# Performance work log

Measured on AMD Instinct MI355X. Metric: run time of the kernel, lower is better.

Reference implementation:

```python
import jax, jax.numpy as jnp
import numpy as np

B, CIN, H, W = 16, 20, 256, 256
WIDTH, M1, M2, NLAYERS, FC_HID, COUT = 64, 16, 16, 4, 128, 20


def setup_inputs() -> dict:
    key = jax.random.key(0)
    ks = jax.random.split(key, 16)
    scale = 1.0 / (WIDTH * WIDTH)  # matches torch: scale * rand(..., cfloat)
    u = lambda k, s: scale * jax.random.uniform(k, s, dtype=jnp.float32)
    n = lambda k, s: 0.05 * jax.random.normal(k, s, dtype=jnp.float32)
    return {
        "x": jax.random.normal(ks[0], (B, CIN, H, W), dtype=jnp.float32),
        # complex spectral weights stored as real/imag pairs, stacked over 4 layers
        "spec_w1r": u(ks[1], (NLAYERS, WIDTH, WIDTH, M1, M2)),
        "spec_w1i": u(ks[2], (NLAYERS, WIDTH, WIDTH, M1, M2)),
        "spec_w2r": u(ks[3], (NLAYERS, WIDTH, WIDTH, M1, M2)),
        "spec_w2i": u(ks[4], (NLAYERS, WIDTH, WIDTH, M1, M2)),
        # 1x1 conv weights (out, in) and biases, stacked over 4 layers
        "pw_w": n(ks[5], (NLAYERS, WIDTH, WIDTH)),
        "pw_b": n(ks[6], (NLAYERS, WIDTH)),
        "fc0_w": n(ks[7], (WIDTH, CIN)),
        "fc0_b": n(ks[8], (WIDTH,)),
        "fc1_w": n(ks[9], (FC_HID, WIDTH)),
        "fc1_b": n(ks[10], (FC_HID,)),
        "fc2_w": n(ks[11], (COUT, FC_HID)),
        "fc2_b": n(ks[12], (COUT,)),
    }


def _spectral_conv(h, w1, w2):
    # h: (B, WIDTH, H, W) real; w1,w2: (WIDTH, WIDTH, M1, M2) complex
    b, c, hh, ww = h.shape
    x_ft = jnp.fft.rfft2(h)  # (B, WIDTH, H, W//2+1) complex64
    top = jnp.einsum('bixy,ioxy->boxy', x_ft[:, :, :M1, :M2], w1)
    bot = jnp.einsum('bixy,ioxy->boxy', x_ft[:, :, -M1:, :M2], w2)
    out_ft = jnp.zeros((b, c, hh, ww // 2 + 1), dtype=jnp.complex64)
    out_ft = out_ft.at[:, :, :M1, :M2].set(top).at[:, :, -M1:, :M2].set(bot)
    return jnp.fft.irfft2(out_ft, s=(hh, ww))


def reference(x, spec_w1r, spec_w1i, spec_w2r, spec_w2i, pw_w, pw_b,
              fc0_w, fc0_b, fc1_w, fc1_b, fc2_w, fc2_b):
    gelu = lambda t: jax.nn.gelu(t, approximate=False)  # torch F.gelu default = erf
    # lift: permute to channels-last, Linear(20->width), back to channels-first
    h = jnp.einsum('bchw,dc->bdhw', x, fc0_w) + fc0_b[None, :, None, None]
    for i in range(NLAYERS):
        w1 = spec_w1r[i] + 1j * spec_w1i[i]
        w2 = spec_w2r[i] + 1j * spec_w2i[i]
        x1 = _spectral_conv(h, w1, w2)
        x2 = jnp.einsum('bihw,oi->bohw', h, pw_w[i]) + pw_b[i][None, :, None, None]
        h = x1 + x2
        if i < NLAYERS - 1:  # no GELU after the 4th block in the original
            h = gelu(h)
    h = jnp.einsum('bchw,dc->bdhw', h, fc1_w) + fc1_b[None, :, None, None]
    h = gelu(h)
    h = jnp.einsum('bchw,dc->bdhw', h, fc2_w) + fc2_b[None, :, None, None]
    return h  # (B, 20, H, W)
```

## Files before the change

### kernel.cpp

```cpp
#include <hip/hip_runtime.h>
#include <hip/hip_bf16.h>


#define HW_TOT 65536
#define PI2_256 0.024543692606170259758f

__device__ __forceinline__ float gelu_exact(float v) {
    return 0.5f * v * (1.0f + erff(v * 0.70710678118654752440f));
}
__device__ __forceinline__ float gelu_fast(float v) {
    float z  = v * 0.70710678118654752440f;
    float az = fabsf(z);
    float t  = __builtin_amdgcn_rcpf(fmaf(0.3275911f, az, 1.0f));
    float p  = t * (0.254829592f + t * (-0.284496736f + t * (1.421413741f +
               t * (-1.453152027f + t * 1.061405429f))));
    float e  = __expf(-az * az);
    float er = copysignf(1.0f - p * e, z);
    return 0.5f * v * (1.0f + er);
}
#define F4COMP(v, k) ((k)==0?(v).x:(k)==1?(v).y:(k)==2?(v).z:(v).w)

template<int CI, int CO, int WS>
__global__ void __launch_bounds__(256) conv1x1_kernel(
    const float* __restrict__ in, const float* __restrict__ w,
    const float* __restrict__ bias, float* __restrict__ out)
{
    const int b = blockIdx.y;
    const int p = blockIdx.x * 256 + threadIdx.x;
    const float* inp = in + (size_t)b * CI * HW_TOT + p;
    float acc[CO];
#pragma unroll
    for (int o = 0; o < CO; ++o) acc[o] = bias[o];
    for (int ci = 0; ci < CI; ++ci) {
        float hv = inp[(size_t)ci * HW_TOT];
#pragma unroll
        for (int o = 0; o < CO; ++o)
            acc[o] = fmaf(w[o * WS + ci], hv, acc[o]);
    }
    float* op = out + (size_t)b * CO * HW_TOT + p;
#pragma unroll
    for (int o = 0; o < CO; ++o) op[(size_t)o * HW_TOT] = acc[o];
}

__global__ void __launch_bounds__(256) dfty_kernel(
    const float* __restrict__ h, float* __restrict__ T)
{
    __shared__ float As[128][68];
    __shared__ float Wc[64][32];
    __shared__ float cs2[256], sn2[256];
    const int t = threadIdx.x;
    {
        float a = (float)t * PI2_256;
        cs2[t] = cosf(a); sn2[t] = sinf(a);
    }
    __syncthreads();

    const size_t rowbase = (size_t)blockIdx.x * 128;
    const int jg = t & 7, rg = t >> 3;
    float acc[4][4];
#pragma unroll
    for (int k = 0; k < 4; ++k)
#pragma unroll
        for (int q = 0; q < 4; ++q) acc[k][q] = 0.0f;

    for (int yc = 0; yc < 256; yc += 64) {
        if (yc) __syncthreads();
#pragma unroll
        for (int it = 0; it < 8; ++it) {
            int idx = t + 256 * it;
            int rr = idx >> 4, c4 = idx & 15;
            float4 v = *(const float4*)(h + (rowbase + rr) * 256 + yc + c4 * 4);
            *(float4*)&As[rr][c4 * 4] = v;
        }
#pragma unroll
        for (int it = 0; it < 8; ++it) {
            int i = t + 256 * it;
            int yl = i >> 5, j = i & 31, ky = j >> 1;
            int m = ((yc + yl) * ky) & 255;
            Wc[yl][j] = (j & 1) ? -sn2[m] : cs2[m];
        }
        __syncthreads();
#pragma unroll 2
        for (int yy = 0; yy < 64; yy += 4) {
            float4 wv[4], av[4];
#pragma unroll
            for (int q = 0; q < 4; ++q) wv[q] = *(const float4*)&Wc[yy + q][jg * 4];
#pragma unroll
            for (int k = 0; k < 4; ++k) av[k] = *(const float4*)&As[rg + 32 * k][yy];
#pragma unroll
            for (int k = 0; k < 4; ++k)
#pragma unroll
                for (int q = 0; q < 4; ++q) {
                    float a = F4COMP(av[k], q);
                    acc[k][0] = fmaf(a, wv[q].x, acc[k][0]);
                    acc[k][1] = fmaf(a, wv[q].y, acc[k][1]);
                    acc[k][2] = fmaf(a, wv[q].z, acc[k][2]);
                    acc[k][3] = fmaf(a, wv[q].w, acc[k][3]);
                }
        }
    }
#pragma unroll
    for (int k = 0; k < 4; ++k) {
        float4 v = make_float4(acc[k][0], acc[k][1], acc[k][2], acc[k][3]);
        *(float4*)&T[(rowbase + rg + 32 * k) * 32 + jg * 4] = v;
    }
}

__global__ void __launch_bounds__(512) dft2_kernel(
    const float2* __restrict__ T2, float2* __restrict__ X2)
{
    __shared__ float cs[256], sn[256];
    const int t = threadIdx.x;
    if (t < 256) {
        float a = (float)t * PI2_256;
        cs[t] = cosf(a); sn[t] = sinf(a);
    }
    __syncthreads();
    const int bc = blockIdx.x;
    const int ky = t & 15, kxi = t >> 4;
    const int kx = (kxi < 16) ? kxi : (224 + kxi);
    const float2* Tp = T2 + (size_t)bc * 4096 + ky;
    float xr = 0.0f, xi = 0.0f;
    int m = 0;
    for (int x = 0; x < 256; ++x) {
        float2 tv = Tp[(size_t)x * 16];
        float c = cs[m], s = sn[m];
        xr = fmaf(tv.x, c, fmaf(tv.y, s, xr));
        xi = fmaf(tv.y, c, fmaf(-tv.x, s, xi));
        m = (m + kx) & 255;
    }
    X2[(size_t)bc * 512 + t] = make_float2(xr, xi);
}

__global__ void __launch_bounds__(512) mix_kernel(
    const float2* __restrict__ X2, float2* __restrict__ Y2,
    const float* __restrict__ w1r, const float* __restrict__ w1i,
    const float* __restrict__ w2r, const float* __restrict__ w2i, int layer)
{
    const int bo = blockIdx.x;
    const int b = bo >> 6, o = bo & 63;
    const int t = threadIdx.x;
    const int ky = t & 15, kxi = t >> 4;
    const bool top = (kxi < 16);
    const int kxm = top ? kxi : (kxi - 16);
    const float* wr = top ? w1r : w2r;
    const float* wi = top ? w1i : w2i;
    float yr = 0.0f, yi = 0.0f;
    for (int i = 0; i < 64; ++i) {
        float2 xv = X2[((size_t)(b * 64 + i) * 32 + kxi) * 16 + ky];
        size_t widx = (((size_t)layer * 64 + i) * 64 + o) * 256 + (kxm * 16 + ky);
        float wrv = wr[widx], wiv = wi[widx];
        yr = fmaf(xv.x, wrv, fmaf(-xv.y, wiv, yr));
        yi = fmaf(xv.x, wiv, fmaf(xv.y, wrv, yi));
    }
    Y2[((size_t)(b * 64 + o) * 32 + kxi) * 16 + ky] = make_float2(yr, yi);
}

__global__ void __launch_bounds__(256) idft1_kernel(
    const float2* __restrict__ Y2, float2* __restrict__ G2)
{
    __shared__ float cs[256], sn[256];
    const int t = threadIdx.x;
    {
        float a = (float)t * PI2_256;
        cs[t] = cosf(a); sn[t] = sinf(a);
    }
    __syncthreads();
    const int bo = blockIdx.x >> 4;
    const int xc = blockIdx.x & 15;
    const int ky = t & 15, xo = t >> 4;
    const int x = xc * 16 + xo;
    const float2* Yp = Y2 + (size_t)bo * 512 + ky;
    float gr = 0.0f, gi = 0.0f;
    for (int kxi = 0; kxi < 32; ++kxi) {
        float2 yv = Yp[(size_t)kxi * 16];
        int kx = (kxi < 16) ? kxi : (224 + kxi);
        int m = (kx * x) & 255;
        float c = cs[m], s = sn[m];
        gr = fmaf(yv.x, c, fmaf(-yv.y, s, gr));
        gi = fmaf(yv.x, s, fmaf(yv.y, c, gi));
    }
    G2[((size_t)bo * 256 + x) * 16 + ky] = make_float2(gr, gi);
}

template<int FUSE>
__global__ void __launch_bounds__(1024, 8) pwcomb_kernel(
    float* __restrict__ h, const float2* __restrict__ G2,
    const float* __restrict__ pw_w, const float* __restrict__ pw_b,
    int layer, int do_gelu,
    const float* __restrict__ w1t, const float* __restrict__ fb1,
    const float* __restrict__ fw2, const float* __restrict__ fb2,
    float* __restrict__ out)
{
    __shared__ float buf[20480];
    float (*hs)[256] = (float (*)[256])buf;
    float (*Wt)[64]  = (float (*)[64])(buf + 16384);
    float (*Gt)[64]  = (float (*)[64])buf;
    float (*Pt)[256] = (float (*)[256])(buf + 2048);
    const int t = threadIdx.x;
    const int b = blockIdx.x >> 8;
    const int x = blockIdx.x & 255;

    const float* wl = pw_w + layer * 4096;
#pragma unroll
    for (int it = 0; it < 4; ++it) {
        int i = t + 1024 * it;
        int o = i & 63, ci = i >> 6;
        Wt[ci][o] = wl[o * 64 + ci];
    }
#pragma unroll
    for (int it = 0; it < 4; ++it) {
        int idx = t + 1024 * it;
        int ci = idx >> 6, c4 = idx & 63;
        float4 v = *(const float4*)(h + ((size_t)(b * 64 + ci) * 256 + x) * 256 + c4 * 4);
        *(float4*)&hs[ci][c4 * 4] = v;
    }
    __syncthreads();

    const int og = t & 15, yg = t >> 4;
    const float* bl = pw_b + layer * 64;
    float acc[4][4];
#pragma unroll
    for (int oj = 0; oj < 4; ++oj) {
        float bv = bl[og * 4 + oj];
#pragma unroll
        for (int yj = 0; yj < 4; ++yj) acc[yj][oj] = bv;
    }
    for (int ci = 0; ci < 64; ++ci) {
        float4 hv = *(const float4*)&hs[ci][yg * 4];
        float4 wv = *(const float4*)&Wt[ci][og * 4];
#pragma unroll
        for (int yj = 0; yj < 4; ++yj) {
            float a = F4COMP(hv, yj);
            acc[yj][0] = fmaf(a, wv.x, acc[yj][0]);
            acc[yj][1] = fmaf(a, wv.y, acc[yj][1]);
            acc[yj][2] = fmaf(a, wv.z, acc[yj][2]);
            acc[yj][3] = fmaf(a, wv.w, acc[yj][3]);
        }
    }
    __syncthreads();

    {
        int o = t >> 4, ky = t & 15;
        float2 g = G2[((size_t)(b * 64 + o) * 256 + x) * 16 + ky];
        Gt[2 * ky][o] = g.x;
        Gt[2 * ky + 1][o] = g.y;
    }
    const float inv = 1.0f / 65536.0f;
#pragma unroll
    for (int it = 0; it < 8; ++it) {
        int i = t + 1024 * it;
        int jp = i >> 8, y = i & 255, ky = jp >> 1;
        int m = (ky * y) & 255;
        float wk = (ky == 0) ? inv : 2.0f * inv;
        float ang = (float)m * PI2_256;
        Pt[jp][y] = (jp & 1) ? -wk * sinf(ang) : wk * cosf(ang);
    }
    __syncthreads();

#pragma unroll 4
    for (int jp = 0; jp < 32; ++jp) {
        float4 pv = *(const float4*)&Pt[jp][yg * 4];
        float4 gv = *(const float4*)&Gt[jp][og * 4];
#pragma unroll
        for (int yj = 0; yj < 4; ++yj) {
            float a = F4COMP(pv, yj);
            acc[yj][0] = fmaf(a, gv.x, acc[yj][0]);
            acc[yj][1] = fmaf(a, gv.y, acc[yj][1]);
            acc[yj][2] = fmaf(a, gv.z, acc[yj][2]);
            acc[yj][3] = fmaf(a, gv.w, acc[yj][3]);
        }
    }

    if (!FUSE) {
#pragma unroll
        for (int oj = 0; oj < 4; ++oj) {
            float4 v;
            v.x = acc[0][oj]; v.y = acc[1][oj]; v.z = acc[2][oj]; v.w = acc[3][oj];
            if (do_gelu) {
                v.x = gelu_fast(v.x); v.y = gelu_fast(v.y);
                v.z = gelu_fast(v.z); v.w = gelu_fast(v.w);
            }
            *(float4*)&h[((size_t)(b * 64 + og * 4 + oj) * 256 + x) * 256 + yg * 4] = v;
        }
        return;
    }

    __syncthreads();
#pragma unroll
    for (int oj = 0; oj < 4; ++oj) {
        float4 v = make_float4(acc[0][oj], acc[1][oj], acc[2][oj], acc[3][oj]);
        *(float4*)&buf[(og * 4 + oj) * 260 + yg * 4] = v;
    }
    __syncthreads();

    const int px = t & 255;
    const int wf = __builtin_amdgcn_readfirstlane(t >> 8);
    float acc2[20];
#pragma unroll
    for (int o = 0; o < 20; ++o) acc2[o] = (wf == 0) ? fb2[o] : 0.0f;

#pragma unroll
    for (int pass = 0; pass < 2; ++pass) {
        const int hd0 = wf * 32 + pass * 16;
        float fa[16];
#pragma unroll
        for (int k = 0; k < 16; ++k) fa[k] = fb1[hd0 + k];
#pragma unroll 2
        for (int ci = 0; ci < 64; ++ci) {
            float a = buf[ci * 260 + px];
            const float* wr = w1t + ci * 128 + hd0;
#pragma unroll
            for (int k = 0; k < 16; ++k) fa[k] = fmaf(wr[k], a, fa[k]);
        }
#pragma unroll
        for (int k = 0; k < 16; ++k) fa[k] = gelu_fast(fa[k]);
#pragma unroll
        for (int o = 0; o < 20; ++o) {
            const float* w2r = fw2 + o * 128 + hd0;
            float s0 = 0.0f, s1 = 0.0f;
#pragma unroll
            for (int k = 0; k < 16; k += 2) {
                s0 = fmaf(w2r[k], fa[k], s0);
                s1 = fmaf(w2r[k + 1], fa[k + 1], s1);
            }
            acc2[o] += s0 + s1;
        }
    }
    __syncthreads();
#pragma unroll
    for (int o = 0; o < 20; ++o) buf[(wf * 20 + o) * 256 + px] = acc2[o];
    __syncthreads();

    float* op = out + (size_t)b * 20 * HW_TOT + x * 256 + px;
#pragma unroll
    for (int j = 0; j < 5; ++j) {
        int o = wf * 5 + j;
        float s = buf[o * 256 + px] + buf[(20 + o) * 256 + px]
                + buf[(40 + o) * 256 + px] + buf[(60 + o) * 256 + px];
        op[(size_t)o * HW_TOT] = s;
    }
}

__global__ void __launch_bounds__(256) transpose_w1_kernel(
    const float* __restrict__ w1, float* __restrict__ w1t)
{
    int i = blockIdx.x * 256 + threadIdx.x;
    int ci = i >> 7, hd = i & 127;
    w1t[i] = w1[hd * 64 + ci];
}

extern "C" void kernel_launch(void* const* d_in, const int* in_sizes, int n_in,
                              void* d_out, int out_size, void* d_ws, size_t ws_size,
                              hipStream_t stream)
{
    const float* x     = (const float*)d_in[0];
    const float* w1r   = (const float*)d_in[1];
    const float* w1i   = (const float*)d_in[2];
    const float* w2r   = (const float*)d_in[3];
    const float* w2i   = (const float*)d_in[4];
    const float* pw_w  = (const float*)d_in[5];
    const float* pw_b  = (const float*)d_in[6];
    const float* fc0_w = (const float*)d_in[7];
    const float* fc0_b = (const float*)d_in[8];
    const float* fc1_w = (const float*)d_in[9];
    const float* fc1_b = (const float*)d_in[10];
    const float* fc2_w = (const float*)d_in[11];
    const float* fc2_b = (const float*)d_in[12];
    float* out = (float*)d_out;
    float* ws  = (float*)d_ws;

    const size_t per_sample_floats = 4849664;
    int CB = 16;
    while (CB > 1 && (size_t)CB * per_sample_floats * 4 > ws_size) CB >>= 1;

    float*  h  = ws;
    float*  T  = ws + (size_t)CB * 4194304;
    float2* T2 = (float2*)T;
    float2* X2 = (float2*)(T + (size_t)CB * 524288);
    float2* Y2 = (float2*)(T + (size_t)CB * 524288 + (size_t)CB * 65536);
    float2* G2 = T2;

    for (int c0 = 0; c0 < 16; c0 += CB) {
        const float* xc = x + (size_t)c0 * 20 * HW_TOT;
        float* oc = out + (size_t)c0 * 20 * HW_TOT;

        conv1x1_kernel<20, 64, 20>
            <<<dim3(256, CB), 256, 0, stream>>>(xc, fc0_w, fc0_b, h);

        for (int l = 0; l < 3; ++l) {
            dfty_kernel <<<CB * 128, 256, 0, stream>>>(h, T);
            dft2_kernel <<<CB * 64, 512, 0, stream>>>(T2, X2);
            mix_kernel  <<<CB * 64, 512, 0, stream>>>(X2, Y2, w1r, w1i, w2r, w2i, l);
            idft1_kernel<<<CB * 64 * 16, 256, 0, stream>>>(Y2, G2);
            pwcomb_kernel<0><<<CB * 256, 1024, 0, stream>>>(
                h, G2, pw_w, pw_b, l, 1,
                nullptr, nullptr, nullptr, nullptr, nullptr);
        }

        dfty_kernel <<<CB * 128, 256, 0, stream>>>(h, T);
        dft2_kernel <<<CB * 64, 512, 0, stream>>>(T2, X2);
        mix_kernel  <<<CB * 64, 512, 0, stream>>>(X2, Y2, w1r, w1i, w2r, w2i, 3);
        idft1_kernel<<<CB * 64 * 16, 256, 0, stream>>>(Y2, G2);
        float* w1t_buf = (float*)Y2;
        transpose_w1_kernel<<<32, 256, 0, stream>>>(fc1_w, w1t_buf);
        pwcomb_kernel<1><<<CB * 256, 1024, 0, stream>>>(
            h, G2, pw_w, pw_b, 3, 0,
            w1t_buf, fc1_b, fc2_w, fc2_b, oc);
    }
}
```

Baseline: 2.457 ms.

## Remap pwcomb threads so each wavefront owns output channels, read weights from global

The pointwise+spectral-combine kernel changes its thread mapping: each wavefront now owns four output channels (wave-uniform index) and each lane owns four y positions. The 1x1 conv weights are then loaded as wave-uniform float4s straight from global memory instead of being transposed into shared memory. The per-element sinf/cosf calls for the inverse-DFT twiddle table are replaced by a 256-entry cos/sin table in shared memory, and the G tile row is padded to 68 to reduce bank conflicts. This aims to cut LDS traffic, shared-memory bank conflicts and transcendental cost, at the price of more global/scalar loads for the weights.

```diff
diff --git a/kernel.cpp b/kernel.cpp
--- a/kernel.cpp
+++ b/kernel.cpp
@@ -194,19 +194,17 @@
 {
     __shared__ float buf[20480];
     float (*hs)[256] = (float (*)[256])buf;
-    float (*Wt)[64]  = (float (*)[64])(buf + 16384);
-    float (*Gt)[64]  = (float (*)[64])buf;
-    float (*Pt)[256] = (float (*)[256])(buf + 2048);
+    float (*Gt)[68]  = (float (*)[68])buf;
+    float (*Pt)[256] = (float (*)[256])(buf + 2176);
+    float* cs2 = buf + 16384;
+    float* sn2 = buf + 16640;
     const int t = threadIdx.x;
     const int b = blockIdx.x >> 8;
     const int x = blockIdx.x & 255;
 
-    const float* wl = pw_w + layer * 4096;
-#pragma unroll
-    for (int it = 0; it < 4; ++it) {
-        int i = t + 1024 * it;
-        int o = i & 63, ci = i >> 6;
-        Wt[ci][o] = wl[o * 64 + ci];
+    if (t < 256) {
+        float a = (float)t * PI2_256;
+        cs2[t] = cosf(a); sn2[t] = sinf(a);
     }
 #pragma unroll
     for (int it = 0; it < 4; ++it) {
@@ -217,25 +215,36 @@
     }
     __syncthreads();
 
-    const int og = t & 15, yg = t >> 4;
+    const int lane = t & 63;
+    const int ow = __builtin_amdgcn_readfirstlane(t >> 6) * 4;
+    const int yq = lane * 4;
+
     const float* bl = pw_b + layer * 64;
     float acc[4][4];
 #pragma unroll
     for (int oj = 0; oj < 4; ++oj) {
-        float bv = bl[og * 4 + oj];
+        float bv = bl[ow + oj];
 #pragma unroll
         for (int yj = 0; yj < 4; ++yj) acc[yj][oj] = bv;
     }
-    for (int ci = 0; ci < 64; ++ci) {
-        float4 hv = *(const float4*)&hs[ci][yg * 4];
-        float4 wv = *(const float4*)&Wt[ci][og * 4];
-#pragma unroll
-        for (int yj = 0; yj < 4; ++yj) {
-            float a = F4COMP(hv, yj);
-            acc[yj][0] = fmaf(a, wv.x, acc[yj][0]);
-            acc[yj][1] = fmaf(a, wv.y, acc[yj][1]);
-            acc[yj][2] = fmaf(a, wv.z, acc[yj][2]);
-            acc[yj][3] = fmaf(a, wv.w, acc[yj][3]);
+    const float* wbase = pw_w + layer * 4096;
+#pragma unroll 2
+    for (int cc = 0; cc < 64; cc += 4) {
+        float4 wva[4];
+#pragma unroll
+        for (int oj = 0; oj < 4; ++oj)
+            wva[oj] = *(const float4*)(wbase + (ow + oj) * 64 + cc);
+#pragma unroll
+        for (int k = 0; k < 4; ++k) {
+            float4 hv = *(const float4*)&hs[cc + k][yq];
+#pragma unroll
+            for (int oj = 0; oj < 4; ++oj) {
+                float w = F4COMP(wva[oj], k);
+                acc[0][oj] = fmaf(hv.x, w, acc[0][oj]);
+                acc[1][oj] = fmaf(hv.y, w, acc[1][oj]);
+                acc[2][oj] = fmaf(hv.z, w, acc[2][oj]);
+                acc[3][oj] = fmaf(hv.w, w, acc[3][oj]);
+            }
         }
     }
     __syncthreads();
@@ -253,15 +262,14 @@
         int jp = i >> 8, y = i & 255, ky = jp >> 1;
         int m = (ky * y) & 255;
         float wk = (ky == 0) ? inv : 2.0f * inv;
-        float ang = (float)m * PI2_256;
-        Pt[jp][y] = (jp & 1) ? -wk * sinf(ang) : wk * cosf(ang);
+        Pt[jp][y] = (jp & 1) ? -wk * sn2[m] : wk * cs2[m];
     }
     __syncthreads();
 
 #pragma unroll 4
     for (int jp = 0; jp < 32; ++jp) {
-        float4 pv = *(const float4*)&Pt[jp][yg * 4];
-        float4 gv = *(const float4*)&Gt[jp][og * 4];
+        float4 pv = *(const float4*)&Pt[jp][yq];
+        float4 gv = *(const float4*)&Gt[jp][ow];
 #pragma unroll
         for (int yj = 0; yj < 4; ++yj) {
             float a = F4COMP(pv, yj);
@@ -275,13 +283,12 @@
     if (!FUSE) {
 #pragma unroll
         for (int oj = 0; oj < 4; ++oj) {
-            float4 v;
-            v.x = acc[0][oj]; v.y = acc[1][oj]; v.z = acc[2][oj]; v.w = acc[3][oj];
+            float4 v = make_float4(acc[0][oj], acc[1][oj], acc[2][oj], acc[3][oj]);
             if (do_gelu) {
                 v.x = gelu_fast(v.x); v.y = gelu_fast(v.y);
                 v.z = gelu_fast(v.z); v.w = gelu_fast(v.w);
             }
-            *(float4*)&h[((size_t)(b * 64 + og * 4 + oj) * 256 + x) * 256 + yg * 4] = v;
+            *(float4*)&h[((size_t)(b * 64 + ow + oj) * 256 + x) * 256 + yq] = v;
         }
         return;
     }
@@ -290,7 +297,7 @@
 #pragma unroll
     for (int oj = 0; oj < 4; ++oj) {
         float4 v = make_float4(acc[0][oj], acc[1][oj], acc[2][oj], acc[3][oj]);
-        *(float4*)&buf[(og * 4 + oj) * 260 + yg * 4] = v;
+        *(float4*)&buf[(ow + oj) * 260 + yq] = v;
     }
     __syncthreads();
 
```

New measurement: 2.128 ms. -13.4%, faster.
